# Performance work log

Hardware: AMD Instinct MI355X
Metric: run time of the kernel (lower is better)

The kernel has to match this reference:

```python
import jax, jax.numpy as jnp
import numpy as np

B, S, E, H = 4, 2048, 256, 8
DK = E // H


def setup_inputs() -> dict:
    key = jax.random.key(0)
    ks = jax.random.split(key, 12)
    glorot = lambda k, shape: jax.random.uniform(k, shape, jnp.float32, -1.0, 1.0) * jnp.sqrt(6.0 / (shape[0] + shape[1]))
    inp = {
        "q": jax.random.normal(ks[0], (B, S, E), jnp.float32),
        "k": jax.random.normal(ks[1], (B, S, E), jnp.float32),
        "v": jax.random.normal(ks[2], (B, S, E), jnp.float32),
        # causal mask, np.triu(k=1)==0 -> lower triangular including diagonal
        "mask": (jnp.triu(jnp.ones((S, S), jnp.int32), k=1) == 0).astype(jnp.int32)[None, None],
        "Wq": glorot(ks[3], (E, E)), "bq": jnp.zeros((E,), jnp.float32),
        "Wk": glorot(ks[4], (E, E)), "bk": jnp.zeros((E,), jnp.float32),
        "Wv": glorot(ks[5], (E, E)), "bv": jnp.zeros((E,), jnp.float32),
        "Wo": glorot(ks[6], (E, E)), "bo": jnp.zeros((E,), jnp.float32),
        "gammas": glorot(ks[7], (H, 1)).reshape(H, 1, 1),  # xavier init of (H,1,1)
    }
    return inp


def reference(q, k, v, mask, Wq, bq, Wk, bk, Wv, bv, Wo, bo, gammas):
    b, s, e = q.shape
    h = gammas.shape[0]
    dk = e // h
    neg = jnp.float32(-1e32)

    def proj(x, W, bias):
        return (x @ W.T + bias).reshape(b, s, h, dk).transpose(0, 2, 1, 3)  # [B,H,S,dk]

    qh, kh, vh = proj(q, Wq, bq), proj(k, Wk, bk), proj(v, Wv, bv)
    scores = jnp.einsum("bhid,bhjd->bhij", qh, kh) / jnp.sqrt(jnp.float32(dk))  # [B,H,S,S]

    # --- no_grad block: monotonic distance-decay term ---
    maskf = mask.astype(scores.dtype)
    s1 = jax.nn.softmax(jnp.where(mask == 0, neg, scores), axis=-1) * maskf
    s1 = jax.lax.stop_gradient(s1)
    distcum = jnp.cumsum(s1, axis=-1)
    disttotal = jnp.sum(s1, axis=-1, keepdims=True)
    idx = jnp.arange(s)
    pos = jnp.abs(idx[None, :] - idx[:, None]).astype(scores.dtype)[None, None]  # |i-j|
    dist = jnp.sqrt(jnp.clip((disttotal - distcum) * pos, 0.0, None))
    dist = jax.lax.stop_gradient(dist)
    # ----------------------------------------------------

    gamma = -jax.nn.softplus(gammas)[None]                      # [1,H,1,1]
    total_effect = jnp.clip(jnp.exp(dist * gamma), 1e-5, 1e5)
    scores = jnp.where(mask == 0, neg, scores * total_effect)
    attn = jax.nn.softmax(scores, axis=-1)                      # zero_pad=False (mask=1 path)
    out = jnp.einsum("bhij,bhjd->bhid", attn, vh)
    concat = out.transpose(0, 2, 1, 3).reshape(b, s, e)
    return concat @ Wo.T + bo
```

## Files before the change

kernel.cpp:

```cpp
#include <hip/hip_runtime.h>
#include <math.h>

#define B_   4
#define S_   2048
#define E_   256
#define H_   8
#define DK_  32
#define NROWS (B_*S_)

typedef unsigned short ushort_t;
typedef __attribute__((ext_vector_type(8))) short  bf16x8;
typedef __attribute__((ext_vector_type(4))) float  f32x4;

#define LOG2E 1.4426950408889634f
#define QSCALE (0.17677669529663687f * 1.4426950408889634f)

#if __has_builtin(__builtin_amdgcn_exp2f)
#define EXP2F(x) __builtin_amdgcn_exp2f(x)
#else
#define EXP2F(x) exp2f(x)
#endif
#if __has_builtin(__builtin_amdgcn_sqrtf)
#define SQRTF(x) __builtin_amdgcn_sqrtf(x)
#else
#define SQRTF(x) sqrtf(x)
#endif
#if __has_builtin(__builtin_amdgcn_rcpf)
#define RCPF(x) __builtin_amdgcn_rcpf(x)
#else
#define RCPF(x) (1.0f/(x))
#endif

__device__ __forceinline__ ushort_t bf16_rne(float x)
{
    unsigned int u = __float_as_uint(x);
    unsigned int r = u + 0x7FFFu + ((u >> 16) & 1u);
    return (ushort_t)(r >> 16);
}
__device__ __forceinline__ float bf16_to_f(ushort_t h)
{
    return __uint_as_float(((unsigned int)h) << 16);
}

__device__ __forceinline__ float scan16(float x)
{
    x += __int_as_float(__builtin_amdgcn_update_dpp(0, __float_as_int(x), 0x111, 0xF, 0xF, true));
    x += __int_as_float(__builtin_amdgcn_update_dpp(0, __float_as_int(x), 0x112, 0xF, 0xF, true));
    x += __int_as_float(__builtin_amdgcn_update_dpp(0, __float_as_int(x), 0x114, 0xF, 0xF, true));
    x += __int_as_float(__builtin_amdgcn_update_dpp(0, __float_as_int(x), 0x118, 0xF, 0xF, true));
    return x;
}
__device__ __forceinline__ float bcast15(float x)
{
    return __int_as_float(__builtin_amdgcn_ds_swizzle(__float_as_int(x), 0x1F0));
}


__global__ __launch_bounds__(256)
void conv_all(const float* __restrict__ q, const float* __restrict__ k,
              const float* __restrict__ v,
              const float* __restrict__ Wq, const float* __restrict__ Wk,
              const float* __restrict__ Wv, const float* __restrict__ Wo,
              ushort_t* __restrict__ xh, ushort_t* __restrict__ xl,
              ushort_t* __restrict__ wh, ushort_t* __restrict__ wl)
{
    const int z = blockIdx.y;
    const float* src;
    ushort_t *dh, *dl;
    if (z < 3) {
        src = (z == 0) ? q : (z == 1) ? k : v;
        dh = xh + (size_t)z * (NROWS * E_);
        dl = xl + (size_t)z * (NROWS * E_);
    } else {
        if (blockIdx.x >= 16) return;
        src = (z == 3) ? Wq : (z == 4) ? Wk : (z == 5) ? Wv : Wo;
        dh = wh + (size_t)(z - 3) * (E_ * E_);
        dl = wl + (size_t)(z - 3) * (E_ * E_);
    }
    const int n0 = blockIdx.x * 16;
    const int lr = threadIdx.x & 15, kq = threadIdx.x >> 4;
    #pragma unroll
    for (int half = 0; half < 2; half++) {
        const int kk = kq * 8 + half * 128;
        const float* s = src + (size_t)(n0 + lr) * E_ + kk;
        const float4 a = *(const float4*)s;
        const float4 b = *(const float4*)(s + 4);
        const float xs[8] = {a.x, a.y, a.z, a.w, b.x, b.y, b.z, b.w};
        bf16x8 hv, lv;
        #pragma unroll
        for (int e = 0; e < 8; e++) {
            const ushort_t hb = bf16_rne(xs[e]);
            hv[e] = (short)hb;
            lv[e] = (short)bf16_rne(xs[e] - bf16_to_f(hb));
        }
        const size_t o = ((size_t)blockIdx.x * 8 + (kk >> 5)) * 512
                       + ((kk >> 3) & 3) * 128 + lr * 8;
        *(bf16x8*)&dh[o] = hv;
        *(bf16x8*)&dl[o] = lv;
    }
}

__global__ __launch_bounds__(64)
void gemm_frag(const ushort_t* __restrict__ Xh, const ushort_t* __restrict__ Xl,
               const ushort_t* __restrict__ Wh, const ushort_t* __restrict__ Wl,
               const float* __restrict__ bias, int mode, float scale,
               ushort_t* __restrict__ Y1, ushort_t* __restrict__ Y2,
               float* __restrict__ Yf)
{
    const int lane = threadIdx.x;
    const int lr = lane & 15, lq = lane >> 4;
    const int mb = blockIdx.x;
    const int nstrip = blockIdx.y;
    const size_t abase = (size_t)nstrip * 4096 + lane * 8;

    f32x4 acc[4] = {{0,0,0,0},{0,0,0,0},{0,0,0,0},{0,0,0,0}};

    #pragma unroll 2
    for (int kc = 0; kc < 8; kc++) {
        const bf16x8 ahi = *(const bf16x8*)(Xh + abase + kc * 512);
        const bf16x8 alo = *(const bf16x8*)(Xl + abase + kc * 512);
        #pragma unroll
        for (int t = 0; t < 4; t++) {
            const size_t wb = ((size_t)(mb * 4 + t) * 8 + kc) * 512 + lane * 8;
            const bf16x8 bhi = *(const bf16x8*)(Wh + wb);
            const bf16x8 blo = *(const bf16x8*)(Wl + wb);
            acc[t] = __builtin_amdgcn_mfma_f32_16x16x32_bf16(alo, bhi, acc[t], 0, 0, 0);
            acc[t] = __builtin_amdgcn_mfma_f32_16x16x32_bf16(ahi, blo, acc[t], 0, 0, 0);
            acc[t] = __builtin_amdgcn_mfma_f32_16x16x32_bf16(ahi, bhi, acc[t], 0, 0, 0);
        }
    }

    #pragma unroll
    for (int t = 0; t < 4; t++) {
        const int col = mb * 64 + t * 16 + lr;
        const float bt = bias[col];
        if (mode == 0) {
            #pragma unroll
            for (int reg = 0; reg < 4; reg++) {
                const int n = nstrip * 16 + lq * 4 + reg;
                Yf[(size_t)n * E_ + col] = acc[t][reg] + bt;
            }
        } else if (mode == 1) {
            const int h = col >> 5, d = col & 31;
            #pragma unroll
            for (int reg = 0; reg < 4; reg++) {
                const int n  = nstrip * 16 + lq * 4 + reg;
                const int bI = n >> 11, sI = n & (S_ - 1);
                const size_t o = (size_t)(bI * H_ + h) * (S_ * DK_)
                               + (size_t)(sI >> 4) * 512
                               + ((d >> 3) & 3) * 128 + (sI & 15) * 8 + (d & 7);
                const float y = (acc[t][reg] + bt) * scale;
                const ushort_t hb = bf16_rne(y);
                Y1[o] = hb;
                Y2[o] = bf16_rne(y - bf16_to_f(hb));
            }
        } else {
            const int h = col >> 5, d = col & 31;
            #pragma unroll
            for (int reg = 0; reg < 4; reg++) {
                const int n  = nstrip * 16 + lq * 4 + reg;
                const int bI = n >> 11, sI = n & (S_ - 1);
                const size_t o = (size_t)(bI * H_ + h) * (S_ * DK_)
                               + (size_t)((sI >> 5) * 2 + (d >> 4)) * 512
                               + ((sI >> 3) & 3) * 128 + (d & 15) * 8 + (sI & 7);
                Y1[o] = bf16_rne(acc[t][reg] + bt);
            }
        }
    }
}

#define VPAD 72

__device__ __forceinline__ void score_tile(f32x4 (&a)[4],
    const ushort_t* __restrict__ Kbh, const ushort_t* __restrict__ Kbl,
    int jt, const bf16x8& qhi, const bf16x8& qlo, int lane, int lr, int lq,
    bool domask, int i0)
{
    #pragma unroll
    for (int tt = 0; tt < 4; tt++) {
        const size_t ko = (size_t)(jt * 4 + tt) * 512 + lane * 8;
        const bf16x8 khi = *(const bf16x8*)(Kbh + ko);
        const bf16x8 klo = *(const bf16x8*)(Kbl + ko);
        f32x4 v = {0.f, 0.f, 0.f, 0.f};
        v = __builtin_amdgcn_mfma_f32_16x16x32_bf16(qlo, khi, v, 0, 0, 0);
        v = __builtin_amdgcn_mfma_f32_16x16x32_bf16(qhi, klo, v, 0, 0, 0);
        v = __builtin_amdgcn_mfma_f32_16x16x32_bf16(qhi, khi, v, 0, 0, 0);
        a[tt] = v;
    }
    if (domask) {
        #pragma unroll
        for (int tt = 0; tt < 4; tt++)
            #pragma unroll
            for (int r = 0; r < 4; r++) {
                const int irow = i0 + lq * 4 + r;
                const int j    = jt * 64 + tt * 16 + lr;
                if (j > irow) a[tt][r] = -3.0e38f;
            }
    }
}

__global__ __launch_bounds__(256)
void attn_flash(const ushort_t* __restrict__ Qh, const ushort_t* __restrict__ Ql,
                const ushort_t* __restrict__ Kh, const ushort_t* __restrict__ Kl,
                const ushort_t* __restrict__ Vs, const float* __restrict__ gammas,
                ushort_t* __restrict__ Ch, ushort_t* __restrict__ Cl)
{
    __shared__ float sTS[16][36];
    __shared__ __align__(16) ushort_t sP[4][16 * VPAD];
    __shared__ float sO[4][16][32];
    __shared__ float sZ[4][16];

    const int tid  = threadIdx.x;
    const int lane = tid & 63, wv = tid >> 6;
    const int lr   = lane & 15, lq = lane >> 4;
    const int unit = blockIdx.x >> 7;
    const int tq   = 31 - unit;
    const int sub  = blockIdx.x & 127;
    const int bh   = sub & 31;
    const int st   = sub >> 5;
    const int h    = bh & 7, b = bh >> 3;
    const int i0   = tq * 64 + st * 16;

    const size_t hb = (size_t)bh * (S_ * DK_);
    const ushort_t* Kbh = Kh + hb;
    const ushort_t* Kbl = Kl + hb;
    const ushort_t* Vb  = Vs + hb;

    const float g   = gammas[h];
    const float gl2 = -((g > 20.f) ? g : log1pf(__expf(g))) * LOG2E;

    const size_t qoff = hb + (size_t)(i0 >> 4) * 512 + lane * 8;
    const bf16x8 qhi = *(const bf16x8*)(Qh + qoff);
    const bf16x8 qlo = *(const bf16x8*)(Ql + qoff);

    for (int jt = wv; jt <= tq; jt += 4) {
        f32x4 a[4];
        score_tile(a, Kbh, Kbl, jt, qhi, qlo, lane, lr, lq, jt == tq, i0);
        #pragma unroll
        for (int r = 0; r < 4; r++) {
            float rs = (EXP2F(a[0][r]) + EXP2F(a[1][r]))
                     + (EXP2F(a[2][r]) + EXP2F(a[3][r]));
            rs += __shfl_xor(rs, 1); rs += __shfl_xor(rs, 2);
            rs += __shfl_xor(rs, 4); rs += __shfl_xor(rs, 8);
            if (lr == 0) sTS[lq * 4 + r][jt] = rs;
        }
    }
    __syncthreads();

    float z2a[4] = {0.f, 0.f, 0.f, 0.f};
    f32x4 O0 = {0.f,0.f,0.f,0.f}, O1 = {0.f,0.f,0.f,0.f};

    if (wv <= tq) {
        float invZ[4], base[4];
        #pragma unroll
        for (int r = 0; r < 4; r++) {
            const int row = lq * 4 + r;
            float run = 0.f, bs = 0.f;
            for (int t = 0; t <= tq; t++) {
                if (t < wv) bs += sTS[row][t];
                run += sTS[row][t];
            }
            invZ[r] = RCPF(run);
            base[r] = bs;
        }

        ushort_t* sPw = &sP[wv][0];
        for (int jt = wv; jt <= tq; jt += 4) {
            const int j0 = jt * 64;
            f32x4 a[4];
            score_tile(a, Kbh, Kbl, jt, qhi, qlo, lane, lr, lq, jt == tq, i0);

            float sc[4][4], tot[4][4];
            #pragma unroll
            for (int tt = 0; tt < 4; tt++)
                #pragma unroll
                for (int r = 0; r < 4; r++) {
                    const float e = EXP2F(a[tt][r]);
                    const float s = scan16(e);
                    sc[tt][r]  = s;
                    tot[tt][r] = bcast15(s);
                }
            #pragma unroll
            for (int r = 0; r < 4; r++) {
                float run2 = base[r];
                #pragma unroll
                for (int tt = 0; tt < 4; tt++) { sc[tt][r] += run2; run2 += tot[tt][r]; }
            }
            #pragma unroll
            for (int tt = 0; tt < 4; tt++) {
                const int j = j0 + tt * 16 + lr;
                #pragma unroll
                for (int r = 0; r < 4; r++) {
                    const int irow = i0 + lq * 4 + r;
                    const float rest = fmaxf(fmaf(-sc[tt][r], invZ[r], 1.0f), 0.f);
                    const float posf = (float)(irow - j);
                    const float dist = SQRTF(fmaxf(rest * posf, 0.f));
                    const float eff  = fmaxf(EXP2F(gl2 * dist), 1e-5f);
                    const float p2   = EXP2F(a[tt][r] * eff);
                    z2a[r] += p2;
                    sPw[(lq * 4 + r) * VPAD + tt * 16 + lr] = bf16_rne(p2);
                }
            }
            #pragma unroll
            for (int kc = 0; kc < 2; kc++) {
                const bf16x8 pa = *(const bf16x8*)&sPw[lr * VPAD + kc * 32 + lq * 8];
                const size_t vb = (size_t)(((j0 >> 5) + kc) * 2) * 512 + lane * 8;
                const bf16x8 v0 = *(const bf16x8*)(Vb + vb);
                const bf16x8 v1 = *(const bf16x8*)(Vb + vb + 512);
                O0 = __builtin_amdgcn_mfma_f32_16x16x32_bf16(pa, v0, O0, 0, 0, 0);
                O1 = __builtin_amdgcn_mfma_f32_16x16x32_bf16(pa, v1, O1, 0, 0, 0);
            }
            if (jt + 4 <= tq) {
                #pragma unroll
                for (int r = 0; r < 4; r++) {
                    const int row = lq * 4 + r;
                    base[r] += sTS[row][jt] + sTS[row][jt+1] + sTS[row][jt+2] + sTS[row][jt+3];
                }
            }
        }
    }

    #pragma unroll
    for (int r = 0; r < 4; r++) {
        float z = z2a[r];
        z += __shfl_xor(z, 1); z += __shfl_xor(z, 2);
        z += __shfl_xor(z, 4); z += __shfl_xor(z, 8);
        if (lr == 0) sZ[wv][lq * 4 + r] = z;
        sO[wv][lq * 4 + r][lr]      = O0[r];
        sO[wv][lq * 4 + r][16 + lr] = O1[r];
    }
    __syncthreads();

    #pragma unroll
    for (int p = 0; p < 2; p++) {
        const int pid = tid + p * 256;
        const int row = pid >> 5, d = pid & 31;
        const float v = (sO[0][row][d] + sO[1][row][d]) + (sO[2][row][d] + sO[3][row][d]);
        const float z = (sZ[0][row] + sZ[1][row]) + (sZ[2][row] + sZ[3][row]);
        const float y = v * RCPF(z);
        const int nIdx = b * S_ + i0 + row;
        const size_t o = ((size_t)(nIdx >> 4) * 8 + h) * 512
                       + (d >> 3) * 128 + (nIdx & 15) * 8 + (d & 7);
        const ushort_t hbb = bf16_rne(y);
        Ch[o] = hbb;
        Cl[o] = bf16_rne(y - bf16_to_f(hbb));
    }
}

extern "C" void kernel_launch(void* const* d_in, const int* in_sizes, int n_in,
                              void* d_out, int out_size, void* d_ws, size_t ws_size,
                              hipStream_t stream)
{
    const float* q      = (const float*)d_in[0];
    const float* k      = (const float*)d_in[1];
    const float* v      = (const float*)d_in[2];
    const float* Wq     = (const float*)d_in[4];
    const float* bq     = (const float*)d_in[5];
    const float* Wk     = (const float*)d_in[6];
    const float* bk     = (const float*)d_in[7];
    const float* Wv     = (const float*)d_in[8];
    const float* bv     = (const float*)d_in[9];
    const float* Wo     = (const float*)d_in[10];
    const float* bo     = (const float*)d_in[11];
    const float* gammas = (const float*)d_in[12];
    float* out = (float*)d_out;

    const size_t N2 = (size_t)NROWS * E_;
    const size_t WN = (size_t)E_ * E_;

    ushort_t* p   = (ushort_t*)d_ws;
    ushort_t* xh  = p;
    ushort_t* xl  = xh + 3 * N2;
    ushort_t* wh  = xl + 3 * N2;
    ushort_t* wl  = wh + 4 * WN;
    ushort_t* qh  = wl + 4 * WN;
    ushort_t* ql  = qh + N2;
    ushort_t* kh  = ql + N2;
    ushort_t* kl  = kh + N2;
    ushort_t* vt  = kl + N2;
    ushort_t* ch  = xh;
    ushort_t* cl  = xh + N2;

    conv_all<<<dim3(NROWS / 16, 7), 256, 0, stream>>>(q, k, v, Wq, Wk, Wv, Wo,
                                                      xh, xl, wh, wl);

    dim3 ggrd(E_ / 64, NROWS / 16);
    gemm_frag<<<ggrd, 64, 0, stream>>>(xh + 0*N2, xl + 0*N2, wh + 0*WN, wl + 0*WN,
                                       bq, 1, QSCALE, qh, ql, nullptr);
    gemm_frag<<<ggrd, 64, 0, stream>>>(xh + 1*N2, xl + 1*N2, wh + 1*WN, wl + 1*WN,
                                       bk, 1, 1.0f, kh, kl, nullptr);
    gemm_frag<<<ggrd, 64, 0, stream>>>(xh + 2*N2, xl + 2*N2, wh + 2*WN, wl + 2*WN,
                                       bv, 2, 1.0f, vt, nullptr, nullptr);

    attn_flash<<<32 * 32 * 4, 256, 0, stream>>>(qh, ql, kh, kl, vt, gammas, ch, cl);

    gemm_frag<<<ggrd, 64, 0, stream>>>(ch, cl, wh + 3*WN, wl + 3*WN,
                                       bo, 0, 1.0f, nullptr, nullptr, out);
}
```

Measured before the change: 244.2 us.

## Merge QKV projections into one launch with 4-wave blocks and prefetched fragments

The three separate Q/K/V projection GEMM launches become one gemm_qkv kernel that picks the projection with blockIdx.z. Blocks grow from one wave to four waves, each handling its own 16-row strip. The shared inner loop now loads the next k-chunk's A and B fragments before issuing the current MFMAs, a software prefetch meant to hide global load latency. The aim is fewer launches and better latency hiding in the projection GEMMs, at the cost of more registers for the double-buffered fragments; the attention kernel, which likely dominates runtime, is unchanged.

```diff
diff --git a/kernel.cpp b/kernel.cpp
--- a/kernel.cpp
+++ b/kernel.cpp
@@ -100,48 +100,79 @@
     }
 }
 
-__global__ __launch_bounds__(64)
-void gemm_frag(const ushort_t* __restrict__ Xh, const ushort_t* __restrict__ Xl,
-               const ushort_t* __restrict__ Wh, const ushort_t* __restrict__ Wl,
-               const float* __restrict__ bias, int mode, float scale,
-               ushort_t* __restrict__ Y1, ushort_t* __restrict__ Y2,
-               float* __restrict__ Yf)
-{
-    const int lane = threadIdx.x;
+__device__ __forceinline__ void gemm_core(
+    const ushort_t* __restrict__ Ah, const ushort_t* __restrict__ Al,
+    const ushort_t* __restrict__ Bh, const ushort_t* __restrict__ Bl,
+    size_t abase, size_t wbase, f32x4 (&acc)[4])
+{
+    bf16x8 aH = *(const bf16x8*)(Ah + abase);
+    bf16x8 aL = *(const bf16x8*)(Al + abase);
+    bf16x8 bH[4], bL[4];
+    #pragma unroll
+    for (int t = 0; t < 4; t++) {
+        bH[t] = *(const bf16x8*)(Bh + wbase + (size_t)t * 8 * 512);
+        bL[t] = *(const bf16x8*)(Bl + wbase + (size_t)t * 8 * 512);
+    }
+    #pragma unroll
+    for (int kc = 0; kc < 8; kc++) {
+        const int kn = (kc + 1) & 7;
+        bf16x8 aH2 = *(const bf16x8*)(Ah + abase + (size_t)kn * 512);
+        bf16x8 aL2 = *(const bf16x8*)(Al + abase + (size_t)kn * 512);
+        bf16x8 bH2[4], bL2[4];
+        #pragma unroll
+        for (int t = 0; t < 4; t++) {
+            bH2[t] = *(const bf16x8*)(Bh + wbase + (size_t)(t * 8 + kn) * 512);
+            bL2[t] = *(const bf16x8*)(Bl + wbase + (size_t)(t * 8 + kn) * 512);
+        }
+        #pragma unroll
+        for (int t = 0; t < 4; t++) {
+            acc[t] = __builtin_amdgcn_mfma_f32_16x16x32_bf16(aL, bH[t], acc[t], 0, 0, 0);
+            acc[t] = __builtin_amdgcn_mfma_f32_16x16x32_bf16(aH, bL[t], acc[t], 0, 0, 0);
+            acc[t] = __builtin_amdgcn_mfma_f32_16x16x32_bf16(aH, bH[t], acc[t], 0, 0, 0);
+        }
+        aH = aH2; aL = aL2;
+        #pragma unroll
+        for (int t = 0; t < 4; t++) { bH[t] = bH2[t]; bL[t] = bL2[t]; }
+    }
+}
+
+__global__ __launch_bounds__(256)
+void gemm_qkv(const ushort_t* __restrict__ Xh, const ushort_t* __restrict__ Xl,
+              const ushort_t* __restrict__ Wh, const ushort_t* __restrict__ Wl,
+              const float* __restrict__ bqp, const float* __restrict__ bkp,
+              const float* __restrict__ bvp,
+              ushort_t* __restrict__ Qh, ushort_t* __restrict__ Ql,
+              ushort_t* __restrict__ Kh, ushort_t* __restrict__ Kl,
+              ushort_t* __restrict__ Vt)
+{
+    const size_t N2 = (size_t)NROWS * E_;
+    const size_t WN = (size_t)E_ * E_;
+    const int z = blockIdx.z;
+    const ushort_t* Ah = Xh + (size_t)z * N2;
+    const ushort_t* Al = Xl + (size_t)z * N2;
+    const ushort_t* Bh = Wh + (size_t)z * WN;
+    const ushort_t* Bl = Wl + (size_t)z * WN;
+    const float* bias = (z == 0) ? bqp : (z == 1) ? bkp : bvp;
+    const float scale = (z == 0) ? QSCALE : 1.0f;
+
+    const int lane = threadIdx.x & 63, wv = threadIdx.x >> 6;
     const int lr = lane & 15, lq = lane >> 4;
     const int mb = blockIdx.x;
-    const int nstrip = blockIdx.y;
+    const int nstrip = blockIdx.y * 4 + wv;
     const size_t abase = (size_t)nstrip * 4096 + lane * 8;
+    const size_t wbase = (size_t)mb * (4 * 8 * 512) + lane * 8;
 
     f32x4 acc[4] = {{0,0,0,0},{0,0,0,0},{0,0,0,0},{0,0,0,0}};
-
-    #pragma unroll 2
-    for (int kc = 0; kc < 8; kc++) {
-        const bf16x8 ahi = *(const bf16x8*)(Xh + abase + kc * 512);
-        const bf16x8 alo = *(const bf16x8*)(Xl + abase + kc * 512);
-        #pragma unroll
-        for (int t = 0; t < 4; t++) {
-            const size_t wb = ((size_t)(mb * 4 + t) * 8 + kc) * 512 + lane * 8;
-            const bf16x8 bhi = *(const bf16x8*)(Wh + wb);
-            const bf16x8 blo = *(const bf16x8*)(Wl + wb);
-            acc[t] = __builtin_amdgcn_mfma_f32_16x16x32_bf16(alo, bhi, acc[t], 0, 0, 0);
-            acc[t] = __builtin_amdgcn_mfma_f32_16x16x32_bf16(ahi, blo, acc[t], 0, 0, 0);
-            acc[t] = __builtin_amdgcn_mfma_f32_16x16x32_bf16(ahi, bhi, acc[t], 0, 0, 0);
-        }
-    }
+    gemm_core(Ah, Al, Bh, Bl, abase, wbase, acc);
 
     #pragma unroll
     for (int t = 0; t < 4; t++) {
         const int col = mb * 64 + t * 16 + lr;
         const float bt = bias[col];
-        if (mode == 0) {
-            #pragma unroll
-            for (int reg = 0; reg < 4; reg++) {
-                const int n = nstrip * 16 + lq * 4 + reg;
-                Yf[(size_t)n * E_ + col] = acc[t][reg] + bt;
-            }
-        } else if (mode == 1) {
-            const int h = col >> 5, d = col & 31;
+        const int h = col >> 5, d = col & 31;
+        if (z <= 1) {
+            ushort_t* Y1 = (z == 0) ? Qh : Kh;
+            ushort_t* Y2 = (z == 0) ? Ql : Kl;
             #pragma unroll
             for (int reg = 0; reg < 4; reg++) {
                 const int n  = nstrip * 16 + lq * 4 + reg;
@@ -155,7 +186,6 @@
                 Y2[o] = bf16_rne(y - bf16_to_f(hb));
             }
         } else {
-            const int h = col >> 5, d = col & 31;
             #pragma unroll
             for (int reg = 0; reg < 4; reg++) {
                 const int n  = nstrip * 16 + lq * 4 + reg;
@@ -163,8 +193,35 @@
                 const size_t o = (size_t)(bI * H_ + h) * (S_ * DK_)
                                + (size_t)((sI >> 5) * 2 + (d >> 4)) * 512
                                + ((sI >> 3) & 3) * 128 + (d & 15) * 8 + (sI & 7);
-                Y1[o] = bf16_rne(acc[t][reg] + bt);
-            }
+                Vt[o] = bf16_rne(acc[t][reg] + bt);
+            }
+        }
+    }
+}
+
+__global__ __launch_bounds__(256)
+void gemm_out(const ushort_t* __restrict__ Xh, const ushort_t* __restrict__ Xl,
+              const ushort_t* __restrict__ Wh, const ushort_t* __restrict__ Wl,
+              const float* __restrict__ bias, float* __restrict__ Yf)
+{
+    const int lane = threadIdx.x & 63, wv = threadIdx.x >> 6;
+    const int lr = lane & 15, lq = lane >> 4;
+    const int mb = blockIdx.x;
+    const int nstrip = blockIdx.y * 4 + wv;
+    const size_t abase = (size_t)nstrip * 4096 + lane * 8;
+    const size_t wbase = (size_t)mb * (4 * 8 * 512) + lane * 8;
+
+    f32x4 acc[4] = {{0,0,0,0},{0,0,0,0},{0,0,0,0},{0,0,0,0}};
+    gemm_core(Xh, Xl, Wh, Wl, abase, wbase, acc);
+
+    #pragma unroll
+    for (int t = 0; t < 4; t++) {
+        const int col = mb * 64 + t * 16 + lr;
+        const float bt = bias[col];
+        #pragma unroll
+        for (int reg = 0; reg < 4; reg++) {
+            const int n = nstrip * 16 + lq * 4 + reg;
+            Yf[(size_t)n * E_ + col] = acc[t][reg] + bt;
         }
     }
 }
@@ -384,16 +441,11 @@
     conv_all<<<dim3(NROWS / 16, 7), 256, 0, stream>>>(q, k, v, Wq, Wk, Wv, Wo,
                                                       xh, xl, wh, wl);
 
-    dim3 ggrd(E_ / 64, NROWS / 16);
-    gemm_frag<<<ggrd, 64, 0, stream>>>(xh + 0*N2, xl + 0*N2, wh + 0*WN, wl + 0*WN,
-                                       bq, 1, QSCALE, qh, ql, nullptr);
-    gemm_frag<<<ggrd, 64, 0, stream>>>(xh + 1*N2, xl + 1*N2, wh + 1*WN, wl + 1*WN,
-                                       bk, 1, 1.0f, kh, kl, nullptr);
-    gemm_frag<<<ggrd, 64, 0, stream>>>(xh + 2*N2, xl + 2*N2, wh + 2*WN, wl + 2*WN,
-                                       bv, 2, 1.0f, vt, nullptr, nullptr);
+    gemm_qkv<<<dim3(E_ / 64, NROWS / 64, 3), 256, 0, stream>>>(
+        xh, xl, wh, wl, bq, bk, bv, qh, ql, kh, kl, vt);
 
     attn_flash<<<32 * 32 * 4, 256, 0, stream>>>(qh, ql, kh, kl, vt, gammas, ch, cl);
 
-    gemm_frag<<<ggrd, 64, 0, stream>>>(ch, cl, wh + 3*WN, wl + 3*WN,
-                                       bo, 0, 1.0f, nullptr, nullptr, out);
-}
+    gemm_out<<<dim3(E_ / 64, NROWS / 64), 256, 0, stream>>>(
+        ch, cl, wh + 3 * WN, wl + 3 * WN, bo, out);
+}
```

Measured after the change: 236.2 us. -3.3%, faster.
